# Kernel tuning notes

Measured on AMD Instinct MI355X. Metric: run time of the kernel, lower is better.

The kernel has to match this reference:

```python
import jax, jax.numpy as jnp
import numpy as np

N = 2048      # total nodes across all graphs
G = 16        # number of graphs
IN = 16       # input_dim
D = 256       # hidden_dim (d_model)
NH = 8        # num_heads
HD = D // NH  # head_dim
FF = 4 * D    # dim_feedforward
L = 4         # num_layers
LAT = 32      # latent_dim
BH = D // 2   # beta_head hidden
LN_EPS = 1e-5


def setup_inputs() -> dict:
    key = jax.random.key(0)
    ks = jax.random.split(key, 32)

    def w(k, shape, fan_in):
        return jax.random.normal(k, shape, jnp.float32) * (1.0 / np.sqrt(fan_in))

    inp = {
        "x": jax.random.normal(ks[0], (N, IN), jnp.float32),
        "coords": jax.random.normal(ks[1], (N, 3), jnp.float32),
        "batch": jnp.sort(jax.random.randint(ks[2], (N,), 0, G)).astype(jnp.int32),
        # input projection
        "Wi": w(ks[3], (IN, D), IN), "bi": jnp.zeros((D,), jnp.float32),
        # per-layer transformer params, stacked on leading layer dim
        "qkv_w": w(ks[4], (L, D, 3 * D), D), "qkv_b": jnp.zeros((L, 3 * D), jnp.float32),
        "out_w": w(ks[5], (L, D, D), D),     "out_b": jnp.zeros((L, D), jnp.float32),
        "ff1_w": w(ks[6], (L, D, FF), D),    "ff1_b": jnp.zeros((L, FF), jnp.float32),
        "ff2_w": w(ks[7], (L, FF, D), FF),   "ff2_b": jnp.zeros((L, D), jnp.float32),
        "ln1_s": jnp.ones((L, D), jnp.float32), "ln1_b": jnp.zeros((L, D), jnp.float32),
        "ln2_s": jnp.ones((L, D), jnp.float32), "ln2_b": jnp.zeros((L, D), jnp.float32),
        # heads
        "lat_w": w(ks[8], (D, LAT), D), "lat_b": jnp.zeros((LAT,), jnp.float32),
        "b1_w": w(ks[9], (D, BH), D),   "b1_b": jnp.zeros((BH,), jnp.float32),
        "b2_w": w(ks[10], (BH, 1), BH), "b2_b": jnp.zeros((1,), jnp.float32),
    }
    return inp


def _layer_norm(h, s, b):
    m = jnp.mean(h, axis=-1, keepdims=True)
    v = jnp.mean(jnp.square(h - m), axis=-1, keepdims=True)
    return (h - m) * jax.lax.rsqrt(v + LN_EPS) * s + b


def _forward(x, batch, Wi, bi, qkv_w, qkv_b, out_w, out_b, ff1_w, ff1_b,
             ff2_w, ff2_b, ln1_s, ln1_b, ln2_s, ln2_b, lat_w, lat_b,
             b1_w, b1_b, b2_w, b2_b):
    n = x.shape[0]
    h = x @ Wi + bi  # [N, D]
    # the per-graph python loop in torch == block-diagonal attention mask
    attn_bias = jnp.where(batch[:, None] == batch[None, :], 0.0, -1e9).astype(h.dtype)  # [N, N]
    scale = 1.0 / np.sqrt(HD)
    for l in range(L):
        qkv = h @ qkv_w[l] + qkv_b[l]                 # [N, 3D]
        q, k, v = jnp.split(qkv, 3, axis=-1)
        q = q.reshape(n, NH, HD)
        k = k.reshape(n, NH, HD)
        v = v.reshape(n, NH, HD)
        scores = jnp.einsum('nhd,mhd->hnm', q, k) * scale + attn_bias[None]  # [H, N, N]
        a = jax.nn.softmax(scores, axis=-1)
        o = jnp.einsum('hnm,mhd->nhd', a, v).reshape(n, D)
        o = o @ out_w[l] + out_b[l]
        h = _layer_norm(h + o, ln1_s[l], ln1_b[l])     # post-norm (torch default)
        f = jax.nn.relu(h @ ff1_w[l] + ff1_b[l]) @ ff2_w[l] + ff2_b[l]
        h = _layer_norm(h + f, ln2_s[l], ln2_b[l])
    lat = h @ lat_w + lat_b                            # [N, LAT]
    norm = jnp.maximum(jnp.linalg.norm(lat, axis=-1, keepdims=True), 1e-12)
    lat = lat / norm * np.sqrt(LAT)
    beta = jax.nn.sigmoid(jax.nn.relu(h @ b1_w + b1_b) @ b2_w + b2_b)  # [N, 1]
    beta = jnp.clip(beta, 1e-6, 1.0 - 1e-6)
    return beta, lat


def reference(x, coords, batch, Wi, bi, qkv_w, qkv_b, out_w, out_b,
              ff1_w, ff1_b, ff2_w, ff2_b, ln1_s, ln1_b, ln2_s, ln2_b,
              lat_w, lat_b, b1_w, b1_b, b2_w, b2_b):
    # coords is accepted (signature fidelity) but unused in the original forward
    del coords
    return _forward(x, batch, Wi, bi, qkv_w, qkv_b, out_w, out_b, ff1_w, ff1_b,
                    ff2_w, ff2_b, ln1_s, ln1_b, ln2_s, ln2_b, lat_w, lat_b,
                    b1_w, b1_b, b2_w, b2_b)
```

## Files before the change

kernel.cpp:

```cpp
#include <hip/hip_runtime.h>
#include <hip/hip_bf16.h>

typedef __attribute__((ext_vector_type(8))) short bf16x8;
typedef __attribute__((ext_vector_type(4))) float f32x4;

__device__ inline float wave_sum64(float v) {
#pragma unroll
  for (int m = 32; m >= 1; m >>= 1) v += __shfl_xor(v, m, 64);
  return v;
}
__device__ inline ushort f2bf(float f) {
  uint u = __float_as_uint(f);
  return (ushort)((u + 0x7FFFu + ((u >> 16) & 1u)) >> 16);
}

__global__ __launch_bounds__(256) void pack_weights(
    const float* __restrict__ qkv_w, const float* __restrict__ out_w,
    const float* __restrict__ ff1_w, const float* __restrict__ ff2_w,
    const float* __restrict__ b1_w, const float* __restrict__ lat_w,
    short* __restrict__ qkv_t, short* __restrict__ out_t,
    short* __restrict__ ff1_t, short* __restrict__ ff2_t,
    short* __restrict__ b1_t, short* __restrict__ lat_t,
    const int* __restrict__ batch, int* __restrict__ starts, int* __restrict__ meta) {
  int t = blockIdx.x;
  if (t == 3112) {
    for (int i = threadIdx.x; i < 2048; i += 256) {
      int b = batch[i];
      if (i == 0) {
        for (int g = 0; g <= b; ++g) starts[g] = 0;
      } else {
        int bp = batch[i - 1];
        for (int g = bp + 1; g <= b; ++g) starts[g] = i;
      }
      if (i == 2047) {
        for (int g = b + 1; g <= 16; ++g) starts[g] = 2048;
      }
    }
    __syncthreads();
    if (threadIdx.x == 0) {
      int nt = 0;
      for (int g = 0; g < 16; ++g) {
        const int js = starts[g], je = starts[g + 1];
        for (int q0 = js; q0 < je; q0 += 16) {
          meta[1 + nt * 3] = q0;
          meta[2 + nt * 3] = js;
          meta[3 + nt * 3] = je;
          ++nt;
        }
      }
      meta[0] = nt;
    }
    return;
  }
  const float* src;
  short* dst;
  int Kd, Nd, rem;
  if (t < 768) {
    int l = t / 192; rem = t % 192; Kd = 256; Nd = 768;
    src = qkv_w + (size_t)l * Kd * Nd; dst = qkv_t + (size_t)l * Nd * Kd;
  } else if (t < 1024) {
    t -= 768; int l = t / 64; rem = t % 64; Kd = 256; Nd = 256;
    src = out_w + (size_t)l * Kd * Nd; dst = out_t + (size_t)l * Nd * Kd;
  } else if (t < 2048) {
    t -= 1024; int l = t / 256; rem = t % 256; Kd = 256; Nd = 1024;
    src = ff1_w + (size_t)l * Kd * Nd; dst = ff1_t + (size_t)l * Nd * Kd;
  } else if (t < 3072) {
    t -= 2048; int l = t / 256; rem = t % 256; Kd = 1024; Nd = 256;
    src = ff2_w + (size_t)l * Kd * Nd; dst = ff2_t + (size_t)l * Nd * Kd;
  } else if (t < 3104) {
    rem = t - 3072; Kd = 256; Nd = 128; src = b1_w; dst = b1_t;
  } else {
    rem = t - 3104; Kd = 256; Nd = 32; src = lat_w; dst = lat_t;
  }
  const int ntn = Nd / 32;
  const int kt = rem / ntn, nt = rem % ntn;

  __shared__ float tile[32][33];
  const int tx = threadIdx.x & 31, ty = threadIdx.x >> 5;
#pragma unroll
  for (int r = 0; r < 4; ++r) {
    int k = kt * 32 + ty + r * 8;
    tile[ty + r * 8][tx] = src[(size_t)k * Nd + nt * 32 + tx];
  }
  __syncthreads();
#pragma unroll
  for (int r = 0; r < 4; ++r) {
    int n = nt * 32 + ty + r * 8;
    dst[(size_t)n * Kd + kt * 32 + tx] = (short)f2bf(tile[tx][ty + r * 8]);
  }
}

__global__ __launch_bounds__(256) void inproj_kernel(
    const float* __restrict__ x, const float* __restrict__ Wi,
    const float* __restrict__ bi, float* __restrict__ h, short* __restrict__ hb) {
  __shared__ float xs[16];
  const int i = blockIdx.x, j = threadIdx.x;
  if (j < 16) xs[j] = x[(size_t)i * 16 + j];
  __syncthreads();
  float acc = bi[j];
#pragma unroll
  for (int k = 0; k < 16; ++k) acc += xs[k] * Wi[k * 256 + j];
  h[(size_t)i * 256 + j] = acc;
  hb[(size_t)i * 256 + j] = (short)f2bf(acc);
}

template <int ACT, int OUTBF, int VT>
__global__ __launch_bounds__(256) void gemm_bf16(
    const short* __restrict__ A, const short* __restrict__ Bt,
    const float* __restrict__ bias, float* __restrict__ Cf, short* __restrict__ Cb,
    short* __restrict__ vtg, int M, int N, int K, int kpb) {
  __shared__ short As[64 * 128];
  __shared__ short Bs[64 * 128];

  const int t = threadIdx.x;
  const int bm = blockIdx.y, bn = blockIdx.x, bz = blockIdx.z;
  const int srow = t >> 2, sq = t & 3;
  const int lane = t & 63, wid = t >> 6;
  const int wr = wid >> 1, wc = wid & 1;
  const int fr = lane & 15, fs = lane >> 4;
  const int rx = srow & 7;

  f32x4 acc[2][2];
#pragma unroll
  for (int m = 0; m < 2; ++m)
#pragma unroll
    for (int n = 0; n < 2; ++n) acc[m][n] = (f32x4){0.f, 0.f, 0.f, 0.f};

  const int kbase = bz * kpb;
  const short* ap = A + (size_t)(bm * 64 + srow) * K + kbase;
  const int ng = bn * 64 + srow;
  const short* bp = Bt + (size_t)ng * K + kbase;
  const int ar0 = wr * 32 + fr, ar1 = ar0 + 16;
  const int bc0 = wc * 32 + fr, bc1 = bc0 + 16;

  for (int k0 = 0; k0 < kpb; k0 += 128) {
    bf16x8 av[4], bv[4];
#pragma unroll
    for (int i = 0; i < 4; ++i) av[i] = *(const bf16x8*)(ap + k0 + (sq * 4 + i) * 8);
    if (ng < N) {
#pragma unroll
      for (int i = 0; i < 4; ++i) bv[i] = *(const bf16x8*)(bp + k0 + (sq * 4 + i) * 8);
    } else {
#pragma unroll
      for (int i = 0; i < 4; ++i) bv[i] = (bf16x8){0, 0, 0, 0, 0, 0, 0, 0};
    }
    __syncthreads();
#pragma unroll
    for (int i = 0; i < 4; ++i) {
      const int s = sq * 4 + i;
      *(bf16x8*)(As + srow * 128 + ((s ^ rx) * 8)) = av[i];
      *(bf16x8*)(Bs + srow * 128 + ((s ^ rx) * 8)) = bv[i];
    }
    __syncthreads();
#pragma unroll
    for (int ks = 0; ks < 4; ++ks) {
      const int u = ks * 4 + fs;
      bf16x8 a0 = *(const bf16x8*)(As + ar0 * 128 + ((u ^ (ar0 & 7)) * 8));
      bf16x8 a1 = *(const bf16x8*)(As + ar1 * 128 + ((u ^ (ar1 & 7)) * 8));
      bf16x8 b0 = *(const bf16x8*)(Bs + bc0 * 128 + ((u ^ (bc0 & 7)) * 8));
      bf16x8 b1 = *(const bf16x8*)(Bs + bc1 * 128 + ((u ^ (bc1 & 7)) * 8));
      acc[0][0] = __builtin_amdgcn_mfma_f32_16x16x32_bf16(a0, b0, acc[0][0], 0, 0, 0);
      acc[0][1] = __builtin_amdgcn_mfma_f32_16x16x32_bf16(a0, b1, acc[0][1], 0, 0, 0);
      acc[1][0] = __builtin_amdgcn_mfma_f32_16x16x32_bf16(a1, b0, acc[1][0], 0, 0, 0);
      acc[1][1] = __builtin_amdgcn_mfma_f32_16x16x32_bf16(a1, b1, acc[1][1], 0, 0, 0);
    }
  }

#pragma unroll
  for (int n = 0; n < 2; ++n) {
    const int col = bn * 64 + wc * 32 + n * 16 + fr;
    if (col < N) {
      const float bvv = (bz == 0) ? bias[col] : 0.f;
#pragma unroll
      for (int m = 0; m < 2; ++m) {
        const int rbase = bm * 64 + wr * 32 + m * 16 + fs * 4;
#pragma unroll
        for (int j = 0; j < 4; ++j) {
          float v = acc[m][n][j] + bvv;
          if (ACT == 1) v = fmaxf(v, 0.f);
          if (OUTBF) {
            Cb[(size_t)(rbase + j) * N + col] = (short)f2bf(v);
          } else {
            Cf[(size_t)(bz * M + rbase + j) * N + col] = v;
          }
        }
      }
    }
  }

  if (VT && bn >= 8) {
    short* tr = As;
    __syncthreads();
#pragma unroll
    for (int n = 0; n < 2; ++n) {
      const int c = wc * 32 + n * 16 + fr;
      const float bvv = bias[bn * 64 + c];
#pragma unroll
      for (int m = 0; m < 2; ++m)
#pragma unroll
        for (int j = 0; j < 4; ++j) {
          const int r = wr * 32 + m * 16 + fs * 4 + j;
          tr[c * 68 + r] = (short)f2bf(acc[m][n][j] + bvv);
        }
    }
    __syncthreads();
    const int tx = t & 63, ty = t >> 6;
    const int d0 = bn * 64 - 512, rb = bm * 64;
#pragma unroll
    for (int r = 0; r < 16; ++r) {
      const int d = ty * 16 + r;
      vtg[(size_t)(d0 + d) * 2048 + rb + tx] = tr[d * 68 + tx];
    }
  }
}

__global__ __launch_bounds__(256) void attn_direct(
    const short* __restrict__ qkv, const short* __restrict__ vtg,
    const int* __restrict__ meta, short* __restrict__ out) {
  const int wid = blockIdx.x * 4 + (threadIdx.x >> 6);
  const int tile = wid >> 3, h = wid & 7;
  if (tile >= meta[0]) return;
  const int lane = threadIdx.x & 63;
  const int fr = lane & 15, fs = lane >> 4;
  const int q0 = meta[1 + tile * 3];
  const int js = meta[2 + tile * 3];
  const int je = meta[3 + tile * 3];
  const int jbase = js & ~15;
  const int njt = (je - jbase + 15) >> 4;
  const float scale = 0.17677669529663687f;

  const int qrow = min(q0 + fr, 2047);
  const bf16x8 qf = *(const bf16x8*)(qkv + (size_t)qrow * 768 + h * 32 + fs * 8);
  const int jeq = (q0 + fr < je) ? je : 0;

  f32x4 s[16];
#pragma unroll
  for (int jt = 0; jt < 16; ++jt)
    s[jt] = (f32x4){-3.0e38f, -3.0e38f, -3.0e38f, -3.0e38f};

#pragma unroll
  for (int jt = 0; jt < 16; ++jt) {
    if (jt < njt) {
      const int krow = min(jbase + jt * 16 + fr, 2047);
      const bf16x8 kf = *(const bf16x8*)(qkv + (size_t)krow * 768 + 256 + h * 32 + fs * 8);
      s[jt] = __builtin_amdgcn_mfma_f32_16x16x32_bf16(
          kf, qf, (f32x4){0.f, 0.f, 0.f, 0.f}, 0, 0, 0);
    }
  }
  float mx = -3.0e38f;
#pragma unroll
  for (int jt = 0; jt < 16; ++jt) {
    if (jt < njt) {
#pragma unroll
      for (int jj = 0; jj < 4; ++jj) {
        const int j = jbase + jt * 16 + fs * 4 + jj;
        const bool valid = (j >= js) && (j < jeq);
        s[jt][jj] = valid ? s[jt][jj] * scale : -3.0e38f;
        mx = fmaxf(mx, s[jt][jj]);
      }
    }
  }
  mx = fmaxf(mx, __shfl_xor(mx, 16, 64));
  mx = fmaxf(mx, __shfl_xor(mx, 32, 64));
  float l = 0.f;
#pragma unroll
  for (int jt = 0; jt < 16; ++jt) {
#pragma unroll
    for (int jj = 0; jj < 4; ++jj) {
      const float p = __expf(s[jt][jj] - mx);
      s[jt][jj] = p;
      l += p;
    }
  }
  l += __shfl_xor(l, 16, 64);
  l += __shfl_xor(l, 32, 64);

  f32x4 oa[2];
  oa[0] = (f32x4){0.f, 0.f, 0.f, 0.f};
  oa[1] = (f32x4){0.f, 0.f, 0.f, 0.f};
#pragma unroll
  for (int p2 = 0; p2 < 8; ++p2) {
    if (p2 * 2 < njt) {
      bf16x8 pa;
      pa[0] = (short)f2bf(s[p2 * 2][0]);     pa[1] = (short)f2bf(s[p2 * 2][1]);
      pa[2] = (short)f2bf(s[p2 * 2][2]);     pa[3] = (short)f2bf(s[p2 * 2][3]);
      pa[4] = (short)f2bf(s[p2 * 2 + 1][0]); pa[5] = (short)f2bf(s[p2 * 2 + 1][1]);
      pa[6] = (short)f2bf(s[p2 * 2 + 1][2]); pa[7] = (short)f2bf(s[p2 * 2 + 1][3]);
      const int jb0 = min(jbase + p2 * 32 + fs * 4, 2044);
      const int jb1 = min(jbase + p2 * 32 + 16 + fs * 4, 2044);
#pragma unroll
      for (int nt = 0; nt < 2; ++nt) {
        const short* vrow = vtg + (size_t)(h * 32 + nt * 16 + fr) * 2048;
        const short4 v0 = *(const short4*)(vrow + jb0);
        const short4 v1 = *(const short4*)(vrow + jb1);
        bf16x8 vf;
        vf[0] = v0.x; vf[1] = v0.y; vf[2] = v0.z; vf[3] = v0.w;
        vf[4] = v1.x; vf[5] = v1.y; vf[6] = v1.z; vf[7] = v1.w;
        oa[nt] = __builtin_amdgcn_mfma_f32_16x16x32_bf16(pa, vf, oa[nt], 0, 0, 0);
      }
    }
  }
#pragma unroll
  for (int jj = 0; jj < 4; ++jj) {
    const float lq = __shfl(l, fs * 4 + jj, 64);
    const int node = q0 + fs * 4 + jj;
    if (node < je) {
      const float inv = 1.f / lq;
      out[(size_t)node * 256 + h * 32 + fr] = (short)f2bf(oa[0][jj] * inv);
      out[(size_t)node * 256 + h * 32 + 16 + fr] = (short)f2bf(oa[1][jj] * inv);
    }
  }
}

template <int P>
__global__ __launch_bounds__(256) void ln_kernel(
    const float* __restrict__ base, const float* __restrict__ delta,
    const float* __restrict__ s, const float* __restrict__ b,
    float* __restrict__ outf, short* __restrict__ outb) {
  const int row = blockIdx.x * 4 + (threadIdx.x >> 6);
  const int lane = threadIdx.x & 63;
  const float4 xa = *(const float4*)(base + (size_t)row * 256 + lane * 4);
  float4 v = xa;
#pragma unroll
  for (int p = 0; p < P; ++p) {
    const float4 xb = *(const float4*)(delta + (size_t)(p * 2048 + row) * 256 + lane * 4);
    v.x += xb.x; v.y += xb.y; v.z += xb.z; v.w += xb.w;
  }
  float sum = wave_sum64(v.x + v.y + v.z + v.w);
  const float mean = sum * (1.f / 256.f);
  float4 d = make_float4(v.x - mean, v.y - mean, v.z - mean, v.w - mean);
  float sq = wave_sum64(d.x * d.x + d.y * d.y + d.z * d.z + d.w * d.w);
  const float rs = rsqrtf(sq * (1.f / 256.f) + 1e-5f);
  const float4 sv = *(const float4*)(s + lane * 4);
  const float4 bv = *(const float4*)(b + lane * 4);
  float4 o = make_float4(d.x * rs * sv.x + bv.x, d.y * rs * sv.y + bv.y,
                         d.z * rs * sv.z + bv.z, d.w * rs * sv.w + bv.w);
  *(float4*)(outf + (size_t)row * 256 + lane * 4) = o;
  short4 ob;
  ob.x = (short)f2bf(o.x); ob.y = (short)f2bf(o.y);
  ob.z = (short)f2bf(o.z); ob.w = (short)f2bf(o.w);
  *(short4*)(outb + (size_t)row * 256 + lane * 4) = ob;
}

__global__ __launch_bounds__(256) void lat_kernel(
    const short* __restrict__ A, const short* __restrict__ Bt,
    const float* __restrict__ bias, float* __restrict__ out) {
  __shared__ short As[64 * 128];
  __shared__ short Bs[64 * 128];
  const int t = threadIdx.x;
  const int bm = blockIdx.x;
  const int srow = t >> 2, sq = t & 3;
  const int lane = t & 63, w = t >> 6;
  const int fr = lane & 15, fs = lane >> 4;
  const int rx = srow & 7;

  f32x4 acc[2];
  acc[0] = (f32x4){0.f, 0.f, 0.f, 0.f};
  acc[1] = (f32x4){0.f, 0.f, 0.f, 0.f};
  const short* ap = A + (size_t)(bm * 64 + srow) * 256;
  const short* bp = Bt + (size_t)srow * 256;
  const int ar = w * 16 + fr;

  for (int k0 = 0; k0 < 256; k0 += 128) {
    bf16x8 av[4], bv[4];
#pragma unroll
    for (int i = 0; i < 4; ++i) av[i] = *(const bf16x8*)(ap + k0 + (sq * 4 + i) * 8);
    if (srow < 32) {
#pragma unroll
      for (int i = 0; i < 4; ++i) bv[i] = *(const bf16x8*)(bp + k0 + (sq * 4 + i) * 8);
    } else {
#pragma unroll
      for (int i = 0; i < 4; ++i) bv[i] = (bf16x8){0, 0, 0, 0, 0, 0, 0, 0};
    }
    __syncthreads();
#pragma unroll
    for (int i = 0; i < 4; ++i) {
      const int s = sq * 4 + i;
      *(bf16x8*)(As + srow * 128 + ((s ^ rx) * 8)) = av[i];
      *(bf16x8*)(Bs + srow * 128 + ((s ^ rx) * 8)) = bv[i];
    }
    __syncthreads();
#pragma unroll
    for (int ks = 0; ks < 4; ++ks) {
      const int u = ks * 4 + fs;
      bf16x8 a0 = *(const bf16x8*)(As + ar * 128 + ((u ^ (ar & 7)) * 8));
      bf16x8 b0 = *(const bf16x8*)(Bs + fr * 128 + ((u ^ (fr & 7)) * 8));
      bf16x8 b1 = *(const bf16x8*)(Bs + (16 + fr) * 128 + ((u ^ ((16 + fr) & 7)) * 8));
      acc[0] = __builtin_amdgcn_mfma_f32_16x16x32_bf16(a0, b0, acc[0], 0, 0, 0);
      acc[1] = __builtin_amdgcn_mfma_f32_16x16x32_bf16(a0, b1, acc[1], 0, 0, 0);
    }
  }
  const float b0v = bias[fr], b1v = bias[16 + fr];
#pragma unroll
  for (int j = 0; j < 4; ++j) {
    const int row = bm * 64 + w * 16 + fs * 4 + j;
    float v0 = acc[0][j] + b0v;
    float v1 = acc[1][j] + b1v;
    float ss = v0 * v0 + v1 * v1;
    ss += __shfl_xor(ss, 1, 64);
    ss += __shfl_xor(ss, 2, 64);
    ss += __shfl_xor(ss, 4, 64);
    ss += __shfl_xor(ss, 8, 64);
    const float inv = 5.656854249492381f / fmaxf(sqrtf(ss), 1e-12f);
    out[(size_t)row * 32 + fr] = v0 * inv;
    out[(size_t)row * 32 + 16 + fr] = v1 * inv;
  }
}

__global__ __launch_bounds__(256) void gemm_beta(
    const short* __restrict__ A, const short* __restrict__ Bt,
    const float* __restrict__ b1b, const float* __restrict__ w2,
    const float* __restrict__ b2b, float* __restrict__ beta) {
  __shared__ float red[64];
  const int t = threadIdx.x, lane = t & 63, w = t >> 6;
  const int fr = lane & 15, fs = lane >> 4;
  const int rb = blockIdx.x * 16;

  f32x4 acc[2];
  acc[0] = (f32x4){0.f, 0.f, 0.f, 0.f};
  acc[1] = (f32x4){0.f, 0.f, 0.f, 0.f};
  const short* ap = A + (size_t)(rb + fr) * 256;
  const short* bp = Bt + (size_t)(w * 32 + fr) * 256;
  for (int k0 = 0; k0 < 256; k0 += 32) {
    const bf16x8 af = *(const bf16x8*)(ap + k0 + fs * 8);
#pragma unroll
    for (int n = 0; n < 2; ++n) {
      const bf16x8 bf = *(const bf16x8*)(bp + (size_t)n * 16 * 256 + k0 + fs * 8);
      acc[n] = __builtin_amdgcn_mfma_f32_16x16x32_bf16(af, bf, acc[n], 0, 0, 0);
    }
  }
  const int c0 = w * 32 + fr, c1 = c0 + 16;
  const float b0 = b1b[c0], b1 = b1b[c1];
  const float w0 = w2[c0], w1 = w2[c1];
  float part[4];
#pragma unroll
  for (int j = 0; j < 4; ++j) {
    const float d0 = fmaxf(acc[0][j] + b0, 0.f);
    const float d1 = fmaxf(acc[1][j] + b1, 0.f);
    part[j] = d0 * w0 + d1 * w1;
#pragma unroll
    for (int m = 1; m <= 8; m <<= 1) part[j] += __shfl_xor(part[j], m, 64);
  }
  if (fr == 0) {
#pragma unroll
    for (int j = 0; j < 4; ++j) red[w * 16 + fs * 4 + j] = part[j];
  }
  __syncthreads();
  if (t < 16) {
    const float S = red[t] + red[16 + t] + red[32 + t] + red[48 + t] + b2b[0];
    float sgm = 1.f / (1.f + __expf(-S));
    sgm = fminf(fmaxf(sgm, 1e-6f), 1.f - 1e-6f);
    beta[rb + t] = sgm;
  }
}

extern "C" void kernel_launch(void* const* d_in, const int* in_sizes, int n_in,
                              void* d_out, int out_size, void* d_ws, size_t ws_size,
                              hipStream_t stream) {
  const int N = 2048, D = 256, FF = 1024, L = 4;

  const float* x     = (const float*)d_in[0];
  const int*   batch = (const int*)d_in[2];
  const float* Wi    = (const float*)d_in[3];
  const float* bi    = (const float*)d_in[4];
  const float* qkv_w = (const float*)d_in[5];
  const float* qkv_b = (const float*)d_in[6];
  const float* out_w = (const float*)d_in[7];
  const float* out_b = (const float*)d_in[8];
  const float* ff1_w = (const float*)d_in[9];
  const float* ff1_b = (const float*)d_in[10];
  const float* ff2_w = (const float*)d_in[11];
  const float* ff2_b = (const float*)d_in[12];
  const float* ln1_s = (const float*)d_in[13];
  const float* ln1_b = (const float*)d_in[14];
  const float* ln2_s = (const float*)d_in[15];
  const float* ln2_b = (const float*)d_in[16];
  const float* lat_w = (const float*)d_in[17];
  const float* lat_b = (const float*)d_in[18];
  const float* b1_w  = (const float*)d_in[19];
  const float* b1_b  = (const float*)d_in[20];
  const float* b2_w  = (const float*)d_in[21];
  const float* b2_b  = (const float*)d_in[22];

  float* ws = (float*)d_ws;
  float* h      = ws;
  float* tmp    = h + (size_t)N * D;
  int*  starts  = (int*)(tmp + (size_t)4 * N * D);
  int*  meta    = starts + 32;
  short* hb     = (short*)(meta + 448);
  short* qkvb   = hb + (size_t)N * D;
  short* attnb  = qkvb + (size_t)N * 3 * D;
  short* ffb    = attnb + (size_t)N * D;
  short* vtg    = ffb + (size_t)N * FF;
  short* qkv_t  = vtg + (size_t)256 * 2048;
  short* out_t  = qkv_t + (size_t)L * 768 * 256;
  short* ff1_t  = out_t + (size_t)L * 256 * 256;
  short* ff2_t  = ff1_t + (size_t)L * 1024 * 256;
  short* b1_t   = ff2_t + (size_t)L * 256 * 1024;
  short* lat_t  = b1_t + (size_t)128 * 256;

  float* beta_out = (float*)d_out;
  float* lat_out  = beta_out + N;

  pack_weights<<<3113, 256, 0, stream>>>(qkv_w, out_w, ff1_w, ff2_w, b1_w, lat_w,
                                         qkv_t, out_t, ff1_t, ff2_t, b1_t, lat_t,
                                         batch, starts, meta);
  inproj_kernel<<<N, 256, 0, stream>>>(x, Wi, bi, h, hb);

  for (int l = 0; l < L; ++l) {
    gemm_bf16<0, 1, 1><<<dim3(12, 32, 1), 256, 0, stream>>>(
        hb, qkv_t + (size_t)l * 768 * 256, qkv_b + (size_t)l * 768,
        nullptr, qkvb, vtg, N, 768, 256, 256);
    attn_direct<<<288, 256, 0, stream>>>(qkvb, vtg, meta, attnb);
    gemm_bf16<0, 0, 0><<<dim3(4, 32, 2), 256, 0, stream>>>(
        attnb, out_t + (size_t)l * 256 * 256, out_b + (size_t)l * 256,
        tmp, nullptr, nullptr, N, 256, 256, 128);
    ln_kernel<2><<<N / 4, 256, 0, stream>>>(h, tmp, ln1_s + (size_t)l * D,
                                            ln1_b + (size_t)l * D, h, hb);
    gemm_bf16<1, 1, 0><<<dim3(16, 32, 1), 256, 0, stream>>>(
        hb, ff1_t + (size_t)l * FF * 256, ff1_b + (size_t)l * FF,
        nullptr, ffb, nullptr, N, FF, 256, 256);
    gemm_bf16<0, 0, 0><<<dim3(4, 32, 4), 256, 0, stream>>>(
        ffb, ff2_t + (size_t)l * 256 * FF, ff2_b + (size_t)l * 256,
        tmp, nullptr, nullptr, N, 256, 1024, 256);
    ln_kernel<4><<<N / 4, 256, 0, stream>>>(h, tmp, ln2_s + (size_t)l * D,
                                            ln2_b + (size_t)l * D, h, hb);
  }

  lat_kernel<<<N / 64, 256, 0, stream>>>(hb, lat_t, lat_b, lat_out);
  gemm_beta<<<128, 256, 0, stream>>>(hb, b1_t, b1_b, b2_w, b2_b, beta_out);
}
```

Before: 213.6 us.

## Fuse layernorm into split-K GEMMs via last-block atomic counter and merge small kernels

Removes the separate layernorm kernels: each split-K output-projection and FF2 GEMM block bumps a per-row-tile atomic counter, and the last block to finish sums the partials, applies the residual and layernorm, and writes h and hb. It also folds the input projection into the weight-packing kernel and merges the latent and beta heads into one launch. The aim is fewer launches and less inter-kernel idle time. The cost is a memset for the counters plus threadfence and atomic traffic, and the last block per tile does serialized LN work.

Result: slower. 449.1 us (+110.2%).

```diff
diff --git a/kernel.cpp b/kernel.cpp
--- a/kernel.cpp
+++ b/kernel.cpp
@@ -14,15 +14,32 @@
   return (ushort)((u + 0x7FFFu + ((u >> 16) & 1u)) >> 16);
 }
 
-__global__ __launch_bounds__(256) void pack_weights(
+__global__ __launch_bounds__(256) void pack_inproj(
     const float* __restrict__ qkv_w, const float* __restrict__ out_w,
     const float* __restrict__ ff1_w, const float* __restrict__ ff2_w,
     const float* __restrict__ b1_w, const float* __restrict__ lat_w,
     short* __restrict__ qkv_t, short* __restrict__ out_t,
     short* __restrict__ ff1_t, short* __restrict__ ff2_t,
     short* __restrict__ b1_t, short* __restrict__ lat_t,
-    const int* __restrict__ batch, int* __restrict__ starts, int* __restrict__ meta) {
+    const int* __restrict__ batch, int* __restrict__ starts, int* __restrict__ meta,
+    const float* __restrict__ x, const float* __restrict__ Wi,
+    const float* __restrict__ bi, float* __restrict__ h, short* __restrict__ hb) {
   int t = blockIdx.x;
+  __shared__ float tile[32][33];
+
+  if (t >= 3113) {
+    const int row = t - 3113;
+    const int j = threadIdx.x;
+    float* xs = &tile[0][0];
+    if (j < 16) xs[j] = x[(size_t)row * 16 + j];
+    __syncthreads();
+    float acc = bi[j];
+#pragma unroll
+    for (int k = 0; k < 16; ++k) acc += xs[k] * Wi[k * 256 + j];
+    h[(size_t)row * 256 + j] = acc;
+    hb[(size_t)row * 256 + j] = (short)f2bf(acc);
+    return;
+  }
   if (t == 3112) {
     for (int i = threadIdx.x; i < 2048; i += 256) {
       int b = batch[i];
@@ -74,8 +91,6 @@
   }
   const int ntn = Nd / 32;
   const int kt = rem / ntn, nt = rem % ntn;
-
-  __shared__ float tile[32][33];
   const int tx = threadIdx.x & 31, ty = threadIdx.x >> 5;
 #pragma unroll
   for (int r = 0; r < 4; ++r) {
@@ -90,27 +105,16 @@
   }
 }
 
-__global__ __launch_bounds__(256) void inproj_kernel(
-    const float* __restrict__ x, const float* __restrict__ Wi,
-    const float* __restrict__ bi, float* __restrict__ h, short* __restrict__ hb) {
-  __shared__ float xs[16];
-  const int i = blockIdx.x, j = threadIdx.x;
-  if (j < 16) xs[j] = x[(size_t)i * 16 + j];
-  __syncthreads();
-  float acc = bi[j];
-#pragma unroll
-  for (int k = 0; k < 16; ++k) acc += xs[k] * Wi[k * 256 + j];
-  h[(size_t)i * 256 + j] = acc;
-  hb[(size_t)i * 256 + j] = (short)f2bf(acc);
-}
-
-template <int ACT, int OUTBF, int VT>
+template <int ACT, int P, int VT>
 __global__ __launch_bounds__(256) void gemm_bf16(
     const short* __restrict__ A, const short* __restrict__ Bt,
     const float* __restrict__ bias, float* __restrict__ Cf, short* __restrict__ Cb,
-    short* __restrict__ vtg, int M, int N, int K, int kpb) {
+    short* __restrict__ vtg, const float* __restrict__ lns,
+    const float* __restrict__ lnb, float* __restrict__ hf, short* __restrict__ hb,
+    int* __restrict__ done, int M, int N, int K, int kpb) {
   __shared__ short As[64 * 128];
   __shared__ short Bs[64 * 128];
+  __shared__ int lastflag;
 
   const int t = threadIdx.x;
   const int bm = blockIdx.y, bn = blockIdx.x, bz = blockIdx.z;
@@ -166,50 +170,98 @@
     }
   }
 
-#pragma unroll
-  for (int n = 0; n < 2; ++n) {
-    const int col = bn * 64 + wc * 32 + n * 16 + fr;
-    if (col < N) {
+  if (P == 0) {
+    if (!(VT && bn >= 8)) {
+#pragma unroll
+      for (int n = 0; n < 2; ++n) {
+        const int col = bn * 64 + wc * 32 + n * 16 + fr;
+        if (col < N) {
+          const float bvv = bias[col];
+#pragma unroll
+          for (int m = 0; m < 2; ++m) {
+            const int rbase = bm * 64 + wr * 32 + m * 16 + fs * 4;
+#pragma unroll
+            for (int j = 0; j < 4; ++j) {
+              float v = acc[m][n][j] + bvv;
+              if (ACT == 1) v = fmaxf(v, 0.f);
+              Cb[(size_t)(rbase + j) * N + col] = (short)f2bf(v);
+            }
+          }
+        }
+      }
+    }
+    if (VT && bn >= 8) {
+      short* tr = As;
+      __syncthreads();
+#pragma unroll
+      for (int n = 0; n < 2; ++n) {
+        const int c = wc * 32 + n * 16 + fr;
+        const float bvv = bias[bn * 64 + c];
+#pragma unroll
+        for (int m = 0; m < 2; ++m)
+#pragma unroll
+          for (int j = 0; j < 4; ++j) {
+            const int r = wr * 32 + m * 16 + fs * 4 + j;
+            tr[c * 68 + r] = (short)f2bf(acc[m][n][j] + bvv);
+          }
+      }
+      __syncthreads();
+      const int tx = t & 63, ty = t >> 6;
+      const int d0 = bn * 64 - 512, rb = bm * 64;
+#pragma unroll
+      for (int r = 0; r < 16; ++r) {
+        const int d = ty * 16 + r;
+        vtg[(size_t)(d0 + d) * 2048 + rb + tx] = tr[d * 68 + tx];
+      }
+    }
+  } else {
+#pragma unroll
+    for (int n = 0; n < 2; ++n) {
+      const int col = bn * 64 + wc * 32 + n * 16 + fr;
       const float bvv = (bz == 0) ? bias[col] : 0.f;
 #pragma unroll
       for (int m = 0; m < 2; ++m) {
         const int rbase = bm * 64 + wr * 32 + m * 16 + fs * 4;
 #pragma unroll
         for (int j = 0; j < 4; ++j) {
-          float v = acc[m][n][j] + bvv;
-          if (ACT == 1) v = fmaxf(v, 0.f);
-          if (OUTBF) {
-            Cb[(size_t)(rbase + j) * N + col] = (short)f2bf(v);
-          } else {
-            Cf[(size_t)(bz * M + rbase + j) * N + col] = v;
-          }
+          Cf[(size_t)(bz * M + rbase + j) * N + col] = acc[m][n][j] + bvv;
         }
       }
     }
-  }
-
-  if (VT && bn >= 8) {
-    short* tr = As;
-    __syncthreads();
-#pragma unroll
-    for (int n = 0; n < 2; ++n) {
-      const int c = wc * 32 + n * 16 + fr;
-      const float bvv = bias[bn * 64 + c];
-#pragma unroll
-      for (int m = 0; m < 2; ++m)
-#pragma unroll
-        for (int j = 0; j < 4; ++j) {
-          const int r = wr * 32 + m * 16 + fs * 4 + j;
-          tr[c * 68 + r] = (short)f2bf(acc[m][n][j] + bvv);
+    __syncthreads();
+    if (t == 0) {
+      __threadfence();
+      const int old = atomicAdd(&done[bm], 1);
+      lastflag = (old == (int)(gridDim.x * gridDim.z) - 1);
+    }
+    __syncthreads();
+    if (lastflag) {
+      __threadfence();
+      const int w = wid;
+      for (int r = 0; r < 16; ++r) {
+        const int row = bm * 64 + w * 16 + r;
+        const int cl = lane * 4;
+        float4 v = *(const float4*)(hf + (size_t)row * 256 + cl);
+#pragma unroll
+        for (int p = 0; p < P; ++p) {
+          const float4 xb = *(const float4*)(Cf + (size_t)(p * M + row) * 256 + cl);
+          v.x += xb.x; v.y += xb.y; v.z += xb.z; v.w += xb.w;
         }
-    }
-    __syncthreads();
-    const int tx = t & 63, ty = t >> 6;
-    const int d0 = bn * 64 - 512, rb = bm * 64;
-#pragma unroll
-    for (int r = 0; r < 16; ++r) {
-      const int d = ty * 16 + r;
-      vtg[(size_t)(d0 + d) * 2048 + rb + tx] = tr[d * 68 + tx];
+        float sum = wave_sum64(v.x + v.y + v.z + v.w);
+        const float mean = sum * (1.f / 256.f);
+        float4 d = make_float4(v.x - mean, v.y - mean, v.z - mean, v.w - mean);
+        float sq = wave_sum64(d.x * d.x + d.y * d.y + d.z * d.z + d.w * d.w);
+        const float rs = rsqrtf(sq * (1.f / 256.f) + 1e-5f);
+        const float4 sv = *(const float4*)(lns + cl);
+        const float4 bvv = *(const float4*)(lnb + cl);
+        float4 o = make_float4(d.x * rs * sv.x + bvv.x, d.y * rs * sv.y + bvv.y,
+                               d.z * rs * sv.z + bvv.z, d.w * rs * sv.w + bvv.w);
+        *(float4*)(hf + (size_t)row * 256 + cl) = o;
+        short4 ob;
+        ob.x = (short)f2bf(o.x); ob.y = (short)f2bf(o.y);
+        ob.z = (short)f2bf(o.z); ob.w = (short)f2bf(o.w);
+        *(short4*)(hb + (size_t)row * 256 + cl) = ob;
+      }
     }
   }
 }
@@ -312,145 +364,112 @@
   }
 }
 
-template <int P>
-__global__ __launch_bounds__(256) void ln_kernel(
-    const float* __restrict__ base, const float* __restrict__ delta,
-    const float* __restrict__ s, const float* __restrict__ b,
-    float* __restrict__ outf, short* __restrict__ outb) {
-  const int row = blockIdx.x * 4 + (threadIdx.x >> 6);
-  const int lane = threadIdx.x & 63;
-  const float4 xa = *(const float4*)(base + (size_t)row * 256 + lane * 4);
-  float4 v = xa;
-#pragma unroll
-  for (int p = 0; p < P; ++p) {
-    const float4 xb = *(const float4*)(delta + (size_t)(p * 2048 + row) * 256 + lane * 4);
-    v.x += xb.x; v.y += xb.y; v.z += xb.z; v.w += xb.w;
-  }
-  float sum = wave_sum64(v.x + v.y + v.z + v.w);
-  const float mean = sum * (1.f / 256.f);
-  float4 d = make_float4(v.x - mean, v.y - mean, v.z - mean, v.w - mean);
-  float sq = wave_sum64(d.x * d.x + d.y * d.y + d.z * d.z + d.w * d.w);
-  const float rs = rsqrtf(sq * (1.f / 256.f) + 1e-5f);
-  const float4 sv = *(const float4*)(s + lane * 4);
-  const float4 bv = *(const float4*)(b + lane * 4);
-  float4 o = make_float4(d.x * rs * sv.x + bv.x, d.y * rs * sv.y + bv.y,
-                         d.z * rs * sv.z + bv.z, d.w * rs * sv.w + bv.w);
-  *(float4*)(outf + (size_t)row * 256 + lane * 4) = o;
-  short4 ob;
-  ob.x = (short)f2bf(o.x); ob.y = (short)f2bf(o.y);
-  ob.z = (short)f2bf(o.z); ob.w = (short)f2bf(o.w);
-  *(short4*)(outb + (size_t)row * 256 + lane * 4) = ob;
-}
-
-__global__ __launch_bounds__(256) void lat_kernel(
-    const short* __restrict__ A, const short* __restrict__ Bt,
-    const float* __restrict__ bias, float* __restrict__ out) {
-  __shared__ short As[64 * 128];
-  __shared__ short Bs[64 * 128];
+__global__ __launch_bounds__(256) void heads_kernel(
+    const short* __restrict__ A, const short* __restrict__ lat_t,
+    const float* __restrict__ lat_b, float* __restrict__ lat_out,
+    const short* __restrict__ b1_t, const float* __restrict__ b1b,
+    const float* __restrict__ w2, const float* __restrict__ b2b,
+    float* __restrict__ beta) {
+  __shared__ short smem[64 * 128 * 2];
   const int t = threadIdx.x;
-  const int bm = blockIdx.x;
-  const int srow = t >> 2, sq = t & 3;
   const int lane = t & 63, w = t >> 6;
   const int fr = lane & 15, fs = lane >> 4;
-  const int rx = srow & 7;
-
-  f32x4 acc[2];
-  acc[0] = (f32x4){0.f, 0.f, 0.f, 0.f};
-  acc[1] = (f32x4){0.f, 0.f, 0.f, 0.f};
-  const short* ap = A + (size_t)(bm * 64 + srow) * 256;
-  const short* bp = Bt + (size_t)srow * 256;
-  const int ar = w * 16 + fr;
-
-  for (int k0 = 0; k0 < 256; k0 += 128) {
-    bf16x8 av[4], bv[4];
-#pragma unroll
-    for (int i = 0; i < 4; ++i) av[i] = *(const bf16x8*)(ap + k0 + (sq * 4 + i) * 8);
-    if (srow < 32) {
-#pragma unroll
-      for (int i = 0; i < 4; ++i) bv[i] = *(const bf16x8*)(bp + k0 + (sq * 4 + i) * 8);
-    } else {
-#pragma unroll
-      for (int i = 0; i < 4; ++i) bv[i] = (bf16x8){0, 0, 0, 0, 0, 0, 0, 0};
-    }
-    __syncthreads();
-#pragma unroll
-    for (int i = 0; i < 4; ++i) {
-      const int s = sq * 4 + i;
-      *(bf16x8*)(As + srow * 128 + ((s ^ rx) * 8)) = av[i];
-      *(bf16x8*)(Bs + srow * 128 + ((s ^ rx) * 8)) = bv[i];
-    }
-    __syncthreads();
-#pragma unroll
-    for (int ks = 0; ks < 4; ++ks) {
-      const int u = ks * 4 + fs;
-      bf16x8 a0 = *(const bf16x8*)(As + ar * 128 + ((u ^ (ar & 7)) * 8));
-      bf16x8 b0 = *(const bf16x8*)(Bs + fr * 128 + ((u ^ (fr & 7)) * 8));
-      bf16x8 b1 = *(const bf16x8*)(Bs + (16 + fr) * 128 + ((u ^ ((16 + fr) & 7)) * 8));
-      acc[0] = __builtin_amdgcn_mfma_f32_16x16x32_bf16(a0, b0, acc[0], 0, 0, 0);
-      acc[1] = __builtin_amdgcn_mfma_f32_16x16x32_bf16(a0, b1, acc[1], 0, 0, 0);
-    }
-  }
-  const float b0v = bias[fr], b1v = bias[16 + fr];
-#pragma unroll
-  for (int j = 0; j < 4; ++j) {
-    const int row = bm * 64 + w * 16 + fs * 4 + j;
-    float v0 = acc[0][j] + b0v;
-    float v1 = acc[1][j] + b1v;
-    float ss = v0 * v0 + v1 * v1;
-    ss += __shfl_xor(ss, 1, 64);
-    ss += __shfl_xor(ss, 2, 64);
-    ss += __shfl_xor(ss, 4, 64);
-    ss += __shfl_xor(ss, 8, 64);
-    const float inv = 5.656854249492381f / fmaxf(sqrtf(ss), 1e-12f);
-    out[(size_t)row * 32 + fr] = v0 * inv;
-    out[(size_t)row * 32 + 16 + fr] = v1 * inv;
-  }
-}
-
-__global__ __launch_bounds__(256) void gemm_beta(
-    const short* __restrict__ A, const short* __restrict__ Bt,
-    const float* __restrict__ b1b, const float* __restrict__ w2,
-    const float* __restrict__ b2b, float* __restrict__ beta) {
-  __shared__ float red[64];
-  const int t = threadIdx.x, lane = t & 63, w = t >> 6;
-  const int fr = lane & 15, fs = lane >> 4;
-  const int rb = blockIdx.x * 16;
-
-  f32x4 acc[2];
-  acc[0] = (f32x4){0.f, 0.f, 0.f, 0.f};
-  acc[1] = (f32x4){0.f, 0.f, 0.f, 0.f};
-  const short* ap = A + (size_t)(rb + fr) * 256;
-  const short* bp = Bt + (size_t)(w * 32 + fr) * 256;
-  for (int k0 = 0; k0 < 256; k0 += 32) {
-    const bf16x8 af = *(const bf16x8*)(ap + k0 + fs * 8);
-#pragma unroll
-    for (int n = 0; n < 2; ++n) {
-      const bf16x8 bf = *(const bf16x8*)(bp + (size_t)n * 16 * 256 + k0 + fs * 8);
-      acc[n] = __builtin_amdgcn_mfma_f32_16x16x32_bf16(af, bf, acc[n], 0, 0, 0);
-    }
-  }
-  const int c0 = w * 32 + fr, c1 = c0 + 16;
-  const float b0 = b1b[c0], b1 = b1b[c1];
-  const float w0 = w2[c0], w1 = w2[c1];
-  float part[4];
-#pragma unroll
-  for (int j = 0; j < 4; ++j) {
-    const float d0 = fmaxf(acc[0][j] + b0, 0.f);
-    const float d1 = fmaxf(acc[1][j] + b1, 0.f);
-    part[j] = d0 * w0 + d1 * w1;
-#pragma unroll
-    for (int m = 1; m <= 8; m <<= 1) part[j] += __shfl_xor(part[j], m, 64);
-  }
-  if (fr == 0) {
-#pragma unroll
-    for (int j = 0; j < 4; ++j) red[w * 16 + fs * 4 + j] = part[j];
-  }
-  __syncthreads();
-  if (t < 16) {
-    const float S = red[t] + red[16 + t] + red[32 + t] + red[48 + t] + b2b[0];
-    float sgm = 1.f / (1.f + __expf(-S));
-    sgm = fminf(fmaxf(sgm, 1e-6f), 1.f - 1e-6f);
-    beta[rb + t] = sgm;
+
+  if (blockIdx.x < 32) {
+    short* As = smem;
+    short* Bs = smem + 64 * 128;
+    const int bm = blockIdx.x;
+    const int srow = t >> 2, sq = t & 3;
+    const int rx = srow & 7;
+    f32x4 acc[2];
+    acc[0] = (f32x4){0.f, 0.f, 0.f, 0.f};
+    acc[1] = (f32x4){0.f, 0.f, 0.f, 0.f};
+    const short* ap = A + (size_t)(bm * 64 + srow) * 256;
+    const short* bp = lat_t + (size_t)srow * 256;
+    const int ar = w * 16 + fr;
+    for (int k0 = 0; k0 < 256; k0 += 128) {
+      bf16x8 av[4], bv[4];
+#pragma unroll
+      for (int i = 0; i < 4; ++i) av[i] = *(const bf16x8*)(ap + k0 + (sq * 4 + i) * 8);
+      if (srow < 32) {
+#pragma unroll
+        for (int i = 0; i < 4; ++i) bv[i] = *(const bf16x8*)(bp + k0 + (sq * 4 + i) * 8);
+      } else {
+#pragma unroll
+        for (int i = 0; i < 4; ++i) bv[i] = (bf16x8){0, 0, 0, 0, 0, 0, 0, 0};
+      }
+      __syncthreads();
+#pragma unroll
+      for (int i = 0; i < 4; ++i) {
+        const int s = sq * 4 + i;
+        *(bf16x8*)(As + srow * 128 + ((s ^ rx) * 8)) = av[i];
+        *(bf16x8*)(Bs + srow * 128 + ((s ^ rx) * 8)) = bv[i];
+      }
+      __syncthreads();
+#pragma unroll
+      for (int ks = 0; ks < 4; ++ks) {
+        const int u = ks * 4 + fs;
+        bf16x8 a0 = *(const bf16x8*)(As + ar * 128 + ((u ^ (ar & 7)) * 8));
+        bf16x8 b0 = *(const bf16x8*)(Bs + fr * 128 + ((u ^ (fr & 7)) * 8));
+        bf16x8 b1 = *(const bf16x8*)(Bs + (16 + fr) * 128 + ((u ^ ((16 + fr) & 7)) * 8));
+        acc[0] = __builtin_amdgcn_mfma_f32_16x16x32_bf16(a0, b0, acc[0], 0, 0, 0);
+        acc[1] = __builtin_amdgcn_mfma_f32_16x16x32_bf16(a0, b1, acc[1], 0, 0, 0);
+      }
+    }
+    const float b0v = lat_b[fr], b1v = lat_b[16 + fr];
+#pragma unroll
+    for (int j = 0; j < 4; ++j) {
+      const int row = bm * 64 + w * 16 + fs * 4 + j;
+      float v0 = acc[0][j] + b0v;
+      float v1 = acc[1][j] + b1v;
+      float ss = v0 * v0 + v1 * v1;
+      ss += __shfl_xor(ss, 1, 64);
+      ss += __shfl_xor(ss, 2, 64);
+      ss += __shfl_xor(ss, 4, 64);
+      ss += __shfl_xor(ss, 8, 64);
+      const float inv = 5.656854249492381f / fmaxf(sqrtf(ss), 1e-12f);
+      lat_out[(size_t)row * 32 + fr] = v0 * inv;
+      lat_out[(size_t)row * 32 + 16 + fr] = v1 * inv;
+    }
+  } else {
+    float* red = (float*)smem;
+    const int rb = (blockIdx.x - 32) * 16;
+    f32x4 acc[2];
+    acc[0] = (f32x4){0.f, 0.f, 0.f, 0.f};
+    acc[1] = (f32x4){0.f, 0.f, 0.f, 0.f};
+    const short* ap = A + (size_t)(rb + fr) * 256;
+    const short* bp = b1_t + (size_t)(w * 32 + fr) * 256;
+    for (int k0 = 0; k0 < 256; k0 += 32) {
+      const bf16x8 af = *(const bf16x8*)(ap + k0 + fs * 8);
+#pragma unroll
+      for (int n = 0; n < 2; ++n) {
+        const bf16x8 bf = *(const bf16x8*)(bp + (size_t)n * 16 * 256 + k0 + fs * 8);
+        acc[n] = __builtin_amdgcn_mfma_f32_16x16x32_bf16(af, bf, acc[n], 0, 0, 0);
+      }
+    }
+    const int c0 = w * 32 + fr, c1 = c0 + 16;
+    const float b0 = b1b[c0], b1 = b1b[c1];
+    const float w0 = w2[c0], w1 = w2[c1];
+    float part[4];
+#pragma unroll
+    for (int j = 0; j < 4; ++j) {
+      const float d0 = fmaxf(acc[0][j] + b0, 0.f);
+      const float d1 = fmaxf(acc[1][j] + b1, 0.f);
+      part[j] = d0 * w0 + d1 * w1;
+#pragma unroll
+      for (int m = 1; m <= 8; m <<= 1) part[j] += __shfl_xor(part[j], m, 64);
+    }
+    if (fr == 0) {
+#pragma unroll
+      for (int j = 0; j < 4; ++j) red[w * 16 + fs * 4 + j] = part[j];
+    }
+    __syncthreads();
+    if (t < 16) {
+      const float S = red[t] + red[16 + t] + red[32 + t] + red[48 + t] + b2b[0];
+      float sgm = 1.f / (1.f + __expf(-S));
+      sgm = fminf(fmaxf(sgm, 1e-6f), 1.f - 1e-6f);
+      beta[rb + t] = sgm;
+    }
   }
 }
 
@@ -485,7 +504,8 @@
   float* ws = (float*)d_ws;
   float* h      = ws;
   float* tmp    = h + (size_t)N * D;
-  int*  starts  = (int*)(tmp + (size_t)4 * N * D);
+  int*  done    = (int*)(tmp + (size_t)4 * N * D);
+  int*  starts  = done + 256;
   int*  meta    = starts + 32;
   short* hb     = (short*)(meta + 448);
   short* qkvb   = hb + (size_t)N * D;
@@ -502,31 +522,32 @@
   float* beta_out = (float*)d_out;
   float* lat_out  = beta_out + N;
 
-  pack_weights<<<3113, 256, 0, stream>>>(qkv_w, out_w, ff1_w, ff2_w, b1_w, lat_w,
-                                         qkv_t, out_t, ff1_t, ff2_t, b1_t, lat_t,
-                                         batch, starts, meta);
-  inproj_kernel<<<N, 256, 0, stream>>>(x, Wi, bi, h, hb);
+  hipMemsetAsync(done, 0, 256 * sizeof(int), stream);
+  pack_inproj<<<3113 + 2048, 256, 0, stream>>>(
+      qkv_w, out_w, ff1_w, ff2_w, b1_w, lat_w,
+      qkv_t, out_t, ff1_t, ff2_t, b1_t, lat_t,
+      batch, starts, meta, x, Wi, bi, h, hb);
 
   for (int l = 0; l < L; ++l) {
-    gemm_bf16<0, 1, 1><<<dim3(12, 32, 1), 256, 0, stream>>>(
+    gemm_bf16<0, 0, 1><<<dim3(12, 32, 1), 256, 0, stream>>>(
         hb, qkv_t + (size_t)l * 768 * 256, qkv_b + (size_t)l * 768,
-        nullptr, qkvb, vtg, N, 768, 256, 256);
+        nullptr, qkvb, vtg, nullptr, nullptr, nullptr, nullptr, nullptr,
+        N, 768, 256, 256);
     attn_direct<<<288, 256, 0, stream>>>(qkvb, vtg, meta, attnb);
-    gemm_bf16<0, 0, 0><<<dim3(4, 32, 2), 256, 0, stream>>>(
+    gemm_bf16<0, 2, 0><<<dim3(4, 32, 2), 256, 0, stream>>>(
         attnb, out_t + (size_t)l * 256 * 256, out_b + (size_t)l * 256,
-        tmp, nullptr, nullptr, N, 256, 256, 128);
-    ln_kernel<2><<<N / 4, 256, 0, stream>>>(h, tmp, ln1_s + (size_t)l * D,
-                                            ln1_b + (size_t)l * D, h, hb);
-    gemm_bf16<1, 1, 0><<<dim3(16, 32, 1), 256, 0, stream>>>(
+        tmp, nullptr, nullptr, ln1_s + (size_t)l * D, ln1_b + (size_t)l * D,
+        h, hb, done + l * 64, N, 256, 256, 128);
+    gemm_bf16<1, 0, 0><<<dim3(16, 32, 1), 256, 0, stream>>>(
         hb, ff1_t + (size_t)l * FF * 256, ff1_b + (size_t)l * FF,
-        nullptr, ffb, nullptr, N, FF, 256, 256);
-    gemm_bf16<0, 0, 0><<<dim3(4, 32, 4), 256, 0, stream>>>(
+        nullptr, ffb, nullptr, nullptr, nullptr, nullptr, nullptr, nullptr,
+        N, FF, 256, 256);
+    gemm_bf16<0, 4, 0><<<dim3(4, 32, 4), 256, 0, stream>>>(
         ffb, ff2_t + (size_t)l * 256 * FF, ff2_b + (size_t)l * 256,
-        tmp, nullptr, nullptr, N, 256, 1024, 256);
-    ln_kernel<4><<<N / 4, 256, 0, stream>>>(h, tmp, ln2_s + (size_t)l * D,
-                                            ln2_b + (size_t)l * D, h, hb);
-  }
-
-  lat_kernel<<<N / 64, 256, 0, stream>>>(hb, lat_t, lat_b, lat_out);
-  gemm_beta<<<128, 256, 0, stream>>>(hb, b1_t, b1_b, b2_w, b2_b, beta_out);
-}
+        tmp, nullptr, nullptr, ln2_s + (size_t)l * D, ln2_b + (size_t)l * D,
+        h, hb, done + l * 64 + 32, N, 256, 1024, 256);
+  }
+
+  heads_kernel<<<160, 256, 0, stream>>>(hb, lat_t, lat_b, lat_out,
+                                        b1_t, b1_b, b2_w, b2_b, beta_out);
+}
```
